# Optimization experiments

Hardware: AMD Instinct MI355X
Metric: run time of the kernel (lower is better)

## Reference

```python
import jax, jax.numpy as jnp
import numpy as np

B, S, D = 2, 2048, 1024
H = 16
HD = D // H

def setup_inputs() -> dict:
    key = jax.random.key(0)
    k1, k2, k3 = jax.random.split(key, 3)
    # xavier-uniform-ish scale for weights
    x = jax.random.normal(k1, (B, S, D), dtype=jnp.float32)
    lim_qkv = np.sqrt(6.0 / (D + 3 * D)).astype(np.float32)
    lim_o = np.sqrt(6.0 / (D + D)).astype(np.float32)
    qkv_w = jax.random.uniform(k2, (3 * D, D), minval=-lim_qkv, maxval=lim_qkv, dtype=jnp.float32)
    o_w = jax.random.uniform(k3, (D, D), minval=-lim_o, maxval=lim_o, dtype=jnp.float32)
    qkv_b = jnp.zeros((3 * D,), dtype=jnp.float32)
    o_b = jnp.zeros((D,), dtype=jnp.float32)
    return {"x": x, "qkv_w": qkv_w, "qkv_b": qkv_b, "o_w": o_w, "o_b": o_b}

def reference(x, qkv_w, qkv_b, o_w, o_b):
    b, s, _ = x.shape
    # qkv projection: Linear(input_dim, 3*embed_dim)
    qkv = jnp.einsum('bsd,ed->bse', x, qkv_w) + qkv_b          # [B,S,3D]
    qkv = qkv.reshape(b, s, H, 3 * HD).transpose(0, 2, 1, 3)    # [B,H,S,3*HD]
    q, k, v = jnp.split(qkv, 3, axis=-1)                        # each [B,H,S,HD]
    scale = 1.0 / np.sqrt(HD).astype(np.float32)
    scores = jnp.einsum('bhqd,bhkd->bhqk', q, k) * scale        # [B,H,S,S]
    attn = jax.nn.softmax(scores, axis=-1)
    vals = jnp.einsum('bhqk,bhkd->bhqd', attn, v)               # [B,H,S,HD]
    vals = vals.transpose(0, 2, 1, 3).reshape(b, s, H * HD)     # [B,S,D]
    o = jnp.einsum('bse,de->bsd', vals, o_w) + o_b              # [B,S,D]
    return o
```

## Files before the change

### kernel.cpp

```cpp
#include <hip/hip_runtime.h>
#include <math.h>
#include <stdint.h>

typedef _Float16 half_t;
typedef _Float16 f16x8 __attribute__((ext_vector_type(8)));
typedef _Float16 f16x4 __attribute__((ext_vector_type(4)));
typedef _Float16 f16x2 __attribute__((ext_vector_type(2)));
typedef float    f32x4 __attribute__((ext_vector_type(4)));
typedef float    f32x16 __attribute__((ext_vector_type(16)));
typedef unsigned int u32x2 __attribute__((ext_vector_type(2)));

__device__ __forceinline__ void gload16(const void* g, void* l) {
    __builtin_amdgcn_global_load_lds(
        (const __attribute__((address_space(1))) void*)(uintptr_t)g,
        (__attribute__((address_space(3))) void*)(uint32_t)(uintptr_t)l,
        16, 0, 0);
}

__device__ __forceinline__ float fast_exp2(float x) {
#if __has_builtin(__builtin_amdgcn_exp2f)
    return __builtin_amdgcn_exp2f(x);
#else
    return exp2f(x);
#endif
}
__device__ __forceinline__ unsigned cvt2h_u32(float a, float b) {
#if __has_builtin(__builtin_amdgcn_cvt_pkrtz)
    union { __fp16 __attribute__((ext_vector_type(2))) s; unsigned d; } u;
    u.s = __builtin_amdgcn_cvt_pkrtz(a, b);
    return u.d;
#else
    union { f16x2 s; unsigned d; } u;
    u.s = (f16x2){ (half_t)a, (half_t)b };
    return u.d;
#endif
}

#define QSCALE 0.18033688011112042f

__global__ __launch_bounds__(256)
void cvt3_kernel(const float* __restrict__ a, half_t* __restrict__ da, int na,
                 const float* __restrict__ b, half_t* __restrict__ db, int nb,
                 const float* __restrict__ c, half_t* __restrict__ dc)
{
    int i = blockIdx.x * 256 + threadIdx.x;
    const float* s; half_t* d; int off;
    if (i < na)           { s = a; d = da; off = i; }
    else if (i < na + nb) { s = b; d = db; off = i - na; }
    else                  { s = c; d = dc; off = i - na - nb; }
    float4 v = reinterpret_cast<const float4*>(s)[off];
    f16x4 h = { (half_t)v.x, (half_t)v.y, (half_t)v.z, (half_t)v.w };
    reinterpret_cast<f16x4*>(d)[off] = h;
}

template<int BM, int BN, int MODE, int MINWG, int DBUF, int MAP>
__global__ __launch_bounds__(256, MINWG)
void gemm_kernel(const half_t* __restrict__ A,
                 const half_t* __restrict__ Bw,
                 const float* __restrict__ bias,
                 void* __restrict__ outp,
                 half_t* __restrict__ kout,
                 half_t* __restrict__ vtout,
                 int N, int K, int nbx)
{
    constexpr int CA = BM / 32, CB = BN / 32;
    constexpr int MW = BM / 2,  NW = BN / 2;
    constexpr int IF = MW / 16, JF = NW / 16;
    constexpr int AE = BM * 64, BE = BN * 64;
    constexpr int NB = DBUF ? 2 : 1;

    __shared__ half_t As[NB * AE];
    __shared__ half_t Bs[NB * BE];

    const int tid  = threadIdx.x;
    const int lane = tid & 63;
    const int w    = tid >> 6;
    const int wm   = w >> 1, wn = w & 1;
    const int lr   = lane & 15, lg = lane >> 4;

    int m0, n0;
    if constexpr (MAP == 1) {
        const int xcd = blockIdx.x & 7;
        const int c   = blockIdx.x >> 3;
        m0 = (xcd * 4 + (c & 3)) * BM;
        n0 = (c >> 2) * BN;
    } else {
        const int nwg = gridDim.x;
        const int cpx = nwg >> 3;
        const int swz = (blockIdx.x & 7) * cpx + (blockIdx.x >> 3);
        m0 = (swz % nbx) * BM;
        n0 = (swz / nbx) * BN;
    }

    const int srow = lane >> 3;
    const int scol = (lane & 7) * 8;

    f32x4 acc[JF][IF] = {};

    if constexpr (!DBUF) {
        for (int k0 = 0; k0 < K; k0 += 64) {
            #pragma unroll
            for (int c = 0; c < CA; ++c) {
                const int chunk = w * CA + c;
                const int row   = chunk * 8 + srow;
                gload16(&A[(size_t)(m0 + row) * K + k0 + scol], &As[chunk * 512]);
            }
            #pragma unroll
            for (int c = 0; c < CB; ++c) {
                const int chunk = w * CB + c;
                const int row   = chunk * 8 + srow;
                gload16(&Bw[(size_t)(n0 + row) * K + k0 + scol], &Bs[chunk * 512]);
            }
            __syncthreads();

            #pragma unroll
            for (int kk = 0; kk < 2; ++kk) {
                f16x8 af[IF], bf[JF];
                #pragma unroll
                for (int i = 0; i < IF; ++i)
                    af[i] = *reinterpret_cast<const f16x8*>(&As[(wm*MW + i*16 + lr) * 64 + kk*32 + lg*8]);
                #pragma unroll
                for (int j = 0; j < JF; ++j)
                    bf[j] = *reinterpret_cast<const f16x8*>(&Bs[(wn*NW + j*16 + lr) * 64 + kk*32 + lg*8]);
                #pragma unroll
                for (int j = 0; j < JF; ++j)
                    #pragma unroll
                    for (int i = 0; i < IF; ++i)
                        acc[j][i] = __builtin_amdgcn_mfma_f32_16x16x32_f16(bf[j], af[i], acc[j][i], 0, 0, 0);
            }
            __syncthreads();
        }
    } else {
        const int NT = K >> 6;
        #pragma unroll
        for (int c = 0; c < CA; ++c) {
            const int chunk = w * CA + c;
            const int row   = chunk * 8 + srow;
            gload16(&A[(size_t)(m0 + row) * K + scol], &As[chunk * 512]);
        }
        #pragma unroll
        for (int c = 0; c < CB; ++c) {
            const int chunk = w * CB + c;
            const int row   = chunk * 8 + srow;
            gload16(&Bw[(size_t)(n0 + row) * K + scol], &Bs[chunk * 512]);
        }
        __syncthreads();

        int cur = 0;
        for (int kt = 0; kt < NT; ++kt) {
            if (kt + 1 < NT) {
                const int k1 = (kt + 1) << 6;
                #pragma unroll
                for (int c = 0; c < CA; ++c) {
                    const int chunk = w * CA + c;
                    const int row   = chunk * 8 + srow;
                    gload16(&A[(size_t)(m0 + row) * K + k1 + scol], &As[(cur ^ 1) * AE + chunk * 512]);
                }
                #pragma unroll
                for (int c = 0; c < CB; ++c) {
                    const int chunk = w * CB + c;
                    const int row   = chunk * 8 + srow;
                    gload16(&Bw[(size_t)(n0 + row) * K + k1 + scol], &Bs[(cur ^ 1) * BE + chunk * 512]);
                }
            }
            #pragma unroll
            for (int kk = 0; kk < 2; ++kk) {
                f16x8 af[IF], bf[JF];
                #pragma unroll
                for (int i = 0; i < IF; ++i)
                    af[i] = *reinterpret_cast<const f16x8*>(&As[cur * AE + (wm*MW + i*16 + lr) * 64 + kk*32 + lg*8]);
                #pragma unroll
                for (int j = 0; j < JF; ++j)
                    bf[j] = *reinterpret_cast<const f16x8*>(&Bs[cur * BE + (wn*NW + j*16 + lr) * 64 + kk*32 + lg*8]);
                #pragma unroll
                for (int j = 0; j < JF; ++j)
                    #pragma unroll
                    for (int i = 0; i < IF; ++i)
                        acc[j][i] = __builtin_amdgcn_mfma_f32_16x16x32_f16(bf[j], af[i], acc[j][i], 0, 0, 0);
            }
            if (kt + 1 < NT) __syncthreads();
            cur ^= 1;
        }
    }

    #pragma unroll
    for (int j = 0; j < JF; ++j) {
        const int nb = n0 + wn*NW + j*16 + lg*4;
        const float4 bv = *reinterpret_cast<const float4*>(&bias[nb]);
        #pragma unroll
        for (int i = 0; i < IF; ++i) {
            const int gm = m0 + wm*MW + i*16 + lr;
            f32x4 v = acc[j][i];
            v[0] += bv.x; v[1] += bv.y; v[2] += bv.z; v[3] += bv.w;
            if (MODE == 1) {
                float4 st = { v[0], v[1], v[2], v[3] };
                *reinterpret_cast<float4*>(&((float*)outp)[(size_t)gm * N + nb]) = st;
            } else {
                const int b = gm >> 11, s = gm & 2047;
                const int h = nb / 192, cc = nb % 192;
                const int t = cc >> 6, d = cc & 63;
                const size_t bh = (size_t)(b * 16 + h);
                if (t == 0) {
                    f16x4 hv = { (half_t)(v[0]*QSCALE), (half_t)(v[1]*QSCALE),
                                 (half_t)(v[2]*QSCALE), (half_t)(v[3]*QSCALE) };
                    *reinterpret_cast<f16x4*>(&((half_t*)outp)[(bh*2048 + s)*64 + d]) = hv;
                } else if (t == 1) {
                    f16x4 hv = { (half_t)v[0], (half_t)v[1], (half_t)v[2], (half_t)v[3] };
                    *reinterpret_cast<f16x4*>(&kout[(bh*2048 + s)*64 + d]) = hv;
                } else {
                    #pragma unroll
                    for (int r = 0; r < 4; ++r)
                        vtout[(bh*64 + d + r)*2048 + s] = (half_t)v[r];
                }
            }
        }
    }
}

__global__ __launch_bounds__(512, 2)
void attn_kernel(const half_t* __restrict__ qb,
                 const half_t* __restrict__ kb,
                 const half_t* __restrict__ vtb,
                 half_t* __restrict__ vals)
{
    __shared__ __attribute__((aligned(16))) char buf[49152];
    half_t* KtH = (half_t*)buf;
    half_t* VtH = (half_t*)(buf + 24576);

    const int tid  = threadIdx.x;
    const int lane = tid & 63;
    const int w    = tid >> 6;
    const int wq   = w & 3;
    const int kh   = w >> 2;
    const int q32  = lane & 31;
    const int hi   = lane >> 5;
    const int i    = blockIdx.x;
    const int bh   = (i & 7) * 4 + ((i >> 3) & 3);
    const int qblk = i >> 5;
    const int b    = bh >> 4, h = bh & 15;
    const size_t base = (size_t)bh * 2048 * 64;
    const int q0 = qblk * 128;
    const int swk = lane & 7;

    f16x8 qf[4];
    {
        const int qr = q0 + wq*32 + q32;
        #pragma unroll
        for (int kd = 0; kd < 4; ++kd)
            qf[kd] = *reinterpret_cast<const f16x8*>(&qb[base + (size_t)qr*64 + kd*16 + hi*8]);
    }

    const int srow = tid >> 3;
    const int ssl  = (tid & 7) ^ (srow & 7);
    const half_t* kg = kb  + base + (size_t)srow * 64   + ssl * 8;
    const half_t* vg = vtb + base + (size_t)srow * 2048 + ssl * 8;
    const int ldst = w * 512;

    f32x16 acco[2] = {};
    float l_run = 0.0f;

    #pragma unroll
    for (int tt = 0; tt < 3; ++tt) {
        gload16(kg + (size_t)tt * 4096, &KtH[tt * 4096 + ldst]);
        gload16(vg + tt * 64,           &VtH[tt * 4096 + ldst]);
    }

    int bi = 0;
    for (int t = 0; t < 32; ++t) {
        const int rem = 31 - t;
        if (rem >= 2)      asm volatile("s_waitcnt vmcnt(4)" ::: "memory");
        else if (rem == 1) asm volatile("s_waitcnt vmcnt(2)" ::: "memory");
        else               asm volatile("s_waitcnt vmcnt(0)" ::: "memory");
        __builtin_amdgcn_s_barrier();
        __builtin_amdgcn_sched_barrier(0);

        const half_t* Kc = &KtH[bi * 4096];
        const half_t* Vc = &VtH[bi * 4096];

        f32x16 accs = {};
        __builtin_amdgcn_s_setprio(1);
        #pragma unroll
        for (int kd = 0; kd < 4; ++kd) {
            const f16x8 kf = *reinterpret_cast<const f16x8*>(
                &Kc[(kh*32 + q32) * 64 + (((kd*2 + hi) ^ swk) << 3)]);
            accs = __builtin_amdgcn_mfma_f32_32x32x16_f16(kf, qf[kd], accs, 0, 0, 0);
        }
        __builtin_amdgcn_s_setprio(0);

        unsigned P2[8];
        float psum = 0.0f;
        #pragma unroll
        for (int p = 0; p < 8; ++p) {
            const float pa = fast_exp2(accs[2*p]);
            const float pb = fast_exp2(accs[2*p+1]);
            psum += pa + pb;
            P2[p] = cvt2h_u32(pa, pb);
        }
        l_run += psum;

        __builtin_amdgcn_s_setprio(1);
        #pragma unroll
        for (int kb2 = 0; kb2 < 2; ++kb2) {
            const u32x2 s0 = __builtin_amdgcn_permlane32_swap(P2[4*kb2+0], P2[4*kb2+2], false, false);
            const u32x2 s1 = __builtin_amdgcn_permlane32_swap(P2[4*kb2+1], P2[4*kb2+3], false, false);
            union { unsigned u[4]; f16x8 v; } pf;
            pf.u[0] = s0[0]; pf.u[1] = s1[0]; pf.u[2] = s0[1]; pf.u[3] = s1[1];
            #pragma unroll
            for (int d2 = 0; d2 < 2; ++d2) {
                const f16x8 vf = *reinterpret_cast<const f16x8*>(
                    &Vc[(d2*32 + q32) * 64 + (((kh*4 + kb2*2 + hi) ^ swk) << 3)]);
                acco[d2] = __builtin_amdgcn_mfma_f32_32x32x16_f16(vf, pf.v, acco[d2], 0, 0, 0);
            }
        }
        __builtin_amdgcn_s_setprio(0);

        __builtin_amdgcn_s_barrier();
        if (t < 29) {
            gload16(kg + (size_t)(t + 3) * 4096, &KtH[bi * 4096 + ldst]);
            gload16(vg + (t + 3) * 64,           &VtH[bi * 4096 + ldst]);
        }
        bi = (bi == 2) ? 0 : bi + 1;
    }

    l_run += __shfl_xor(l_run, 32);

    float* mrg = (float*)buf;
    __syncthreads();
    if (kh == 1) {
        float* dst = &mrg[(wq*64 + lane) * 33];
        #pragma unroll
        for (int d2 = 0; d2 < 2; ++d2)
            #pragma unroll
            for (int r = 0; r < 16; ++r) dst[d2*16 + r] = acco[d2][r];
        dst[32] = l_run;
    }
    __syncthreads();
    if (kh == 0) {
        const float* src = &mrg[(wq*64 + lane) * 33];
        const float inv_l = 1.0f / (l_run + src[32]);
        const int row = b*2048 + q0 + wq*32 + q32;
        #pragma unroll
        for (int d2 = 0; d2 < 2; ++d2) {
            #pragma unroll
            for (int rq = 0; rq < 4; ++rq) {
                const int dbase = d2*32 + rq*8 + hi*4;
                f16x4 hv;
                #pragma unroll
                for (int j = 0; j < 4; ++j) {
                    const int r = rq*4 + j;
                    hv[j] = (half_t)((acco[d2][r] + src[d2*16 + r]) * inv_l);
                }
                *reinterpret_cast<f16x4*>(&vals[(size_t)row*1024 + h*64 + dbase]) = hv;
            }
        }
    }
}

extern "C" void kernel_launch(void* const* d_in, const int* in_sizes, int n_in,
                              void* d_out, int out_size, void* d_ws, size_t ws_size,
                              hipStream_t stream)
{
    const float* x     = (const float*)d_in[0];
    const float* qkv_w = (const float*)d_in[1];
    const float* qkv_b = (const float*)d_in[2];
    const float* o_w   = (const float*)d_in[3];
    const float* o_b   = (const float*)d_in[4];
    float* out = (float*)d_out;

    const size_t M1 = (size_t)1024 * 1024;
    half_t* x16   = (half_t*)d_ws;
    half_t* w16   = x16   + 4 * M1;
    half_t* ow16  = w16   + 3 * M1;
    half_t* qbuf  = ow16  + 1 * M1;
    half_t* kbuf  = qbuf  + 4 * M1;
    half_t* vtbuf = kbuf  + 4 * M1;
    half_t* vals  = vtbuf + 4 * M1;

    cvt3_kernel<<<8192, 256, 0, stream>>>(x, x16, 1048576, qkv_w, w16, 786432, o_w, ow16);
    gemm_kernel<128, 64, 0, 6, 0, 1><<<1536, 256, 0, stream>>>(
        x16, w16, qkv_b, qbuf, kbuf, vtbuf, 3072, 1024, 32);
    attn_kernel<<<512, 512, 0, stream>>>(qbuf, kbuf, vtbuf, vals);
    gemm_kernel<128, 64, 1, 2, 1, 0><<<512, 256, 0, stream>>>(
        vals, ow16, o_b, out, nullptr, nullptr, 1024, 1024, 32);
}
```

Before: 115.8 us.

## XOR-swizzle GEMM LDS tiles and widen QKV GEMM tile to 128x128

Applies an XOR swizzle to the 16-byte column chunks in the LDS A/B tiles, both on the global-to-LDS writes and on the MFMA fragment reads, to cut LDS bank conflicts. It drops the XCD-specific block mapping and uses the generic swizzled mapping for both GEMMs. The QKV projection GEMM moves from 128x64 tiles with 1536 workgroups to 128x128 tiles with 768 workgroups, for more operand reuse at the cost of more registers and lower occupancy.

Measured after the change: 101.8 us. -12.1%, faster.

```diff
diff --git a/kernel.cpp b/kernel.cpp
--- a/kernel.cpp
+++ b/kernel.cpp
@@ -53,7 +53,7 @@
     reinterpret_cast<f16x4*>(d)[off] = h;
 }
 
-template<int BM, int BN, int MODE, int MINWG, int DBUF, int MAP>
+template<int BM, int BN, int MODE, int MINWG, int DBUF>
 __global__ __launch_bounds__(256, MINWG)
 void gemm_kernel(const half_t* __restrict__ A,
                  const half_t* __restrict__ Bw,
@@ -77,23 +77,16 @@
     const int w    = tid >> 6;
     const int wm   = w >> 1, wn = w & 1;
     const int lr   = lane & 15, lg = lane >> 4;
-
-    int m0, n0;
-    if constexpr (MAP == 1) {
-        const int xcd = blockIdx.x & 7;
-        const int c   = blockIdx.x >> 3;
-        m0 = (xcd * 4 + (c & 3)) * BM;
-        n0 = (c >> 2) * BN;
-    } else {
-        const int nwg = gridDim.x;
-        const int cpx = nwg >> 3;
-        const int swz = (blockIdx.x & 7) * cpx + (blockIdx.x >> 3);
-        m0 = (swz % nbx) * BM;
-        n0 = (swz / nbx) * BN;
-    }
+    const int swk  = lr & 7;
+
+    const int nwg = gridDim.x;
+    const int cpx = nwg >> 3;
+    const int swz = (blockIdx.x & 7) * cpx + (blockIdx.x >> 3);
+    const int m0  = (swz % nbx) * BM;
+    const int n0  = (swz / nbx) * BN;
 
     const int srow = lane >> 3;
-    const int scol = (lane & 7) * 8;
+    const int scol = ((lane & 7) ^ srow) * 8;
 
     f32x4 acc[JF][IF] = {};
 
@@ -118,10 +111,12 @@
                 f16x8 af[IF], bf[JF];
                 #pragma unroll
                 for (int i = 0; i < IF; ++i)
-                    af[i] = *reinterpret_cast<const f16x8*>(&As[(wm*MW + i*16 + lr) * 64 + kk*32 + lg*8]);
+                    af[i] = *reinterpret_cast<const f16x8*>(
+                        &As[(wm*MW + i*16 + lr) * 64 + (((kk*4 + lg) ^ swk) << 3)]);
                 #pragma unroll
                 for (int j = 0; j < JF; ++j)
-                    bf[j] = *reinterpret_cast<const f16x8*>(&Bs[(wn*NW + j*16 + lr) * 64 + kk*32 + lg*8]);
+                    bf[j] = *reinterpret_cast<const f16x8*>(
+                        &Bs[(wn*NW + j*16 + lr) * 64 + (((kk*4 + lg) ^ swk) << 3)]);
                 #pragma unroll
                 for (int j = 0; j < JF; ++j)
                     #pragma unroll
@@ -168,10 +163,12 @@
                 f16x8 af[IF], bf[JF];
                 #pragma unroll
                 for (int i = 0; i < IF; ++i)
-                    af[i] = *reinterpret_cast<const f16x8*>(&As[cur * AE + (wm*MW + i*16 + lr) * 64 + kk*32 + lg*8]);
+                    af[i] = *reinterpret_cast<const f16x8*>(
+                        &As[cur * AE + (wm*MW + i*16 + lr) * 64 + (((kk*4 + lg) ^ swk) << 3)]);
                 #pragma unroll
                 for (int j = 0; j < JF; ++j)
-                    bf[j] = *reinterpret_cast<const f16x8*>(&Bs[cur * BE + (wn*NW + j*16 + lr) * 64 + kk*32 + lg*8]);
+                    bf[j] = *reinterpret_cast<const f16x8*>(
+                        &Bs[cur * BE + (wn*NW + j*16 + lr) * 64 + (((kk*4 + lg) ^ swk) << 3)]);
                 #pragma unroll
                 for (int j = 0; j < JF; ++j)
                     #pragma unroll
@@ -377,9 +374,9 @@
     half_t* vals  = vtbuf + 4 * M1;
 
     cvt3_kernel<<<8192, 256, 0, stream>>>(x, x16, 1048576, qkv_w, w16, 786432, o_w, ow16);
-    gemm_kernel<128, 64, 0, 6, 0, 1><<<1536, 256, 0, stream>>>(
+    gemm_kernel<128, 128, 0, 3, 0><<<768, 256, 0, stream>>>(
         x16, w16, qkv_b, qbuf, kbuf, vtbuf, 3072, 1024, 32);
     attn_kernel<<<512, 512, 0, stream>>>(qbuf, kbuf, vtbuf, vals);
-    gemm_kernel<128, 64, 1, 2, 1, 0><<<512, 256, 0, stream>>>(
+    gemm_kernel<128, 64, 1, 2, 1><<<512, 256, 0, stream>>>(
         vals, ow16, o_b, out, nullptr, nullptr, 1024, 1024, 32);
 }
```
